# Kernel tuning notes

Hardware: AMD Instinct MI355X
Metric: run time of the kernel (lower is better)

The kernel has to match this reference:

```python
import jax, jax.numpy as jnp
import numpy as np

LN_EPS = 1e-5


def setup_inputs() -> dict:
    key = jax.random.key(0)
    k1, k2 = jax.random.split(key)
    n, c, t, v = 64, 256, 128, 25
    inner2 = 512  # 2 * hidden_dim * n_heads
    return {
        "x": jax.random.normal(k1, (n, c, t, v), dtype=jnp.float32),
        "ln_gamma": jnp.ones((c,), dtype=jnp.float32),
        "ln_beta": jnp.zeros((c,), dtype=jnp.float32),
        "W": jax.random.normal(k2, (inner2, c), dtype=jnp.float32),
        "b": jnp.zeros((inner2,), dtype=jnp.float32),
        "n_heads": 8,
    }


def reference(x, ln_gamma, ln_beta, W, b, n_heads):
    n, c, t, v = x.shape
    inner2 = W.shape[0]
    d = inner2 // 2 // n_heads  # per-head dim
    scale = d ** (-0.5)

    # n c t v -> n t v c
    y = jnp.transpose(x, (0, 2, 3, 1))
    # LayerNorm over channel dim
    mu = jnp.mean(y, axis=-1, keepdims=True)
    var = jnp.mean(jnp.square(y - mu), axis=-1, keepdims=True)
    y = (y - mu) * jax.lax.rsqrt(var + LN_EPS) * ln_gamma + ln_beta
    # QK projection: (n, t, v, 2*h*d)
    y = jnp.einsum('ntvc,ec->ntve', y, W) + b
    q, k = jnp.split(y, 2, axis=-1)

    def heads(z):
        # (n, t, v, h*d) -> (n*t, h, v, d)
        z = z.reshape(n * t, v, n_heads, d)
        return jnp.transpose(z, (0, 2, 1, 3))

    q, k = heads(q), heads(k)
    dots = jnp.einsum('bhid,bhjd->bhij', q, k) * scale
    attn = jax.nn.softmax(dots, axis=-1).astype(jnp.float32)
    return attn
```

## Files before the change

### kernel.cpp

```cpp
#include <hip/hip_runtime.h>
#include <math.h>
#include <stdint.h>

typedef _Float16 f16x8 __attribute__((ext_vector_type(8)));
typedef float    f32x4 __attribute__((ext_vector_type(4)));

#define NB    8192
#define V_    25
#define KS_   0.25505003938643f

__global__ __launch_bounds__(256)
void prep_w(const float* __restrict__ W, _Float16* __restrict__ ws) {
    int tid  = blockIdx.x * 256 + threadIdx.x;
    int lane = tid & 63;
    int idx  = tid >> 6;
    int C    = idx >> 4;
    int T2   = idx & 15;
    int half = C >> 3, ch = C & 7;
    int l15  = lane & 15, q4 = lane >> 4;
    const float* src = W + (size_t)(half*256 + T2*16 + l15) * 256 + ch*32 + q4*8;
    f16x8 hi, lo;
    #pragma unroll
    for (int j = 0; j < 8; ++j) {
        float w = src[j];
        _Float16 hh = (_Float16)w;
        hi[j] = hh;
        lo[j] = (_Float16)(w - (float)hh);
    }
    char* base = (char*)ws + (size_t)idx * 2048 + lane * 16;
    *(f16x8*)base          = hi;
    *(f16x8*)(base + 1024) = lo;
}

struct __align__(16) SMem {
    union {
        float xbuf[256][36];
        struct {
            _Float16 ysh[32][264];
            _Float16 ysl[32][264];
        } g;
        _Float16 qk[4][2][32][72];
    } u;
    float s_mu[32];
    float s_rs[32];
};

__global__ __launch_bounds__(256, 3)
void fused_ln_qk_attn(const float* __restrict__ x,
                      const float* __restrict__ gamma,
                      const float* __restrict__ beta,
                      const _Float16* __restrict__ wsp,
                      const float* __restrict__ bias,
                      float* __restrict__ out)
{
    __shared__ SMem sm;

    const int tid  = threadIdx.x;
    const int lane = tid & 63;
    const int wv   = tid >> 6;
    const int l15  = lane & 15;
    const int q4   = lane >> 4;
    const int nt   = blockIdx.x;
    const int n    = nt >> 7;
    const int t    = nt & 127;
    const int base = n * 819200 + t * 25;

    float xv[32];
    {
        const float* xr = x + base + tid * 3200;
        #pragma unroll
        for (int v = 0; v < V_; ++v) xv[v] = xr[v];
        #pragma unroll
        for (int v = V_; v < 32; ++v) xv[v] = 0.0f;
        #pragma unroll
        for (int i = 0; i < 8; ++i) {
            float4 f;
            f.x = xv[i*4+0]; f.y = xv[i*4+1]; f.z = xv[i*4+2]; f.w = xv[i*4+3];
            *(float4*)&sm.u.xbuf[tid][i*4] = f;
        }
    }
    __syncthreads();

    {
        const int v = tid >> 3;
        const int j = tid & 7;
        float s1 = 0.0f, s2 = 0.0f;
        #pragma unroll 4
        for (int m = 0; m < 32; ++m) {
            float val = sm.u.xbuf[j + 8*m][v];
            s1 += val; s2 += val * val;
        }
        s1 += __shfl_xor(s1, 1); s2 += __shfl_xor(s2, 1);
        s1 += __shfl_xor(s1, 2); s2 += __shfl_xor(s2, 2);
        s1 += __shfl_xor(s1, 4); s2 += __shfl_xor(s2, 4);
        if (j == 0) {
            if (v < V_) {
                float mu  = s1 * (1.0f/256.0f);
                float var = s2 * (1.0f/256.0f) - mu * mu;
                sm.s_mu[v] = mu;
                sm.s_rs[v] = rsqrtf(var + 1e-5f);
            } else { sm.s_mu[v] = 0.0f; sm.s_rs[v] = 0.0f; }
        }
    }
    __syncthreads();

    {
        const float g  = gamma[tid];
        const float be = beta[tid];
        #pragma unroll
        for (int v = 0; v < V_; ++v) {
            float val = (xv[v] - sm.s_mu[v]) * sm.s_rs[v] * g + be;
            _Float16 h = (_Float16)val;
            sm.u.g.ysh[v][tid] = h;
            sm.u.g.ysl[v][tid] = (_Float16)(val - (float)h);
        }
    }
    __syncthreads();

    float bv[2][4];
    #pragma unroll
    for (int h = 0; h < 2; ++h)
        #pragma unroll
        for (int j = 0; j < 4; ++j)
            bv[h][j] = bias[h*256 + (wv*4 + j)*16 + l15];

    f32x4 acc[2][2][4];
    #pragma unroll
    for (int h = 0; h < 2; ++h)
        #pragma unroll
        for (int m = 0; m < 2; ++m)
            #pragma unroll
            for (int j = 0; j < 4; ++j)
                acc[h][m][j] = (f32x4){0.f, 0.f, 0.f, 0.f};

    const char* bbase = (const char*)wsp + (size_t)lane * 16 + (size_t)(wv*4) * 2048;

    for (int ch = 0; ch < 8; ++ch) {
        const int kb = ch*32 + q4*8;
        f16x8 Ah0 = *(const f16x8*)&sm.u.g.ysh[l15][kb];
        f16x8 Ah1 = *(const f16x8*)&sm.u.g.ysh[16 + l15][kb];
        f16x8 Al0 = *(const f16x8*)&sm.u.g.ysl[l15][kb];
        f16x8 Al1 = *(const f16x8*)&sm.u.g.ysl[16 + l15][kb];
        #pragma unroll
        for (int half = 0; half < 2; ++half) {
            const char* cb = bbase + (size_t)(half*8 + ch) * 16 * 2048;
            #pragma unroll
            for (int j = 0; j < 4; ++j) {
                const char* pj = cb + (size_t)j * 2048;
                f16x8 Bh = *(const f16x8*)pj;
                f16x8 Bl = *(const f16x8*)(pj + 1024);
                acc[half][0][j] = __builtin_amdgcn_mfma_f32_16x16x32_f16(Ah0, Bh, acc[half][0][j], 0, 0, 0);
                acc[half][0][j] = __builtin_amdgcn_mfma_f32_16x16x32_f16(Al0, Bh, acc[half][0][j], 0, 0, 0);
                acc[half][0][j] = __builtin_amdgcn_mfma_f32_16x16x32_f16(Ah0, Bl, acc[half][0][j], 0, 0, 0);
                acc[half][1][j] = __builtin_amdgcn_mfma_f32_16x16x32_f16(Ah1, Bh, acc[half][1][j], 0, 0, 0);
                acc[half][1][j] = __builtin_amdgcn_mfma_f32_16x16x32_f16(Al1, Bh, acc[half][1][j], 0, 0, 0);
                acc[half][1][j] = __builtin_amdgcn_mfma_f32_16x16x32_f16(Ah1, Bl, acc[half][1][j], 0, 0, 0);
            }
        }
    }
    __syncthreads();

    #pragma unroll
    for (int hh = 0; hh < 2; ++hh) {
        _Float16 (*qh)[72] = sm.u.qk[wv][0];
        _Float16 (*ql)[72] = sm.u.qk[wv][1];

        #pragma unroll
        for (int half = 0; half < 2; ++half)
            #pragma unroll
            for (int jj = 0; jj < 2; ++jj) {
                const int  j   = 2*hh + jj;
                const float bb = bv[half][j];
                const int  col = half*32 + jj*16 + l15;
                #pragma unroll
                for (int mt = 0; mt < 2; ++mt)
                    #pragma unroll
                    for (int r = 0; r < 4; ++r) {
                        const int row = mt*16 + q4*4 + r;
                        float val  = acc[half][mt][j][r] + bb;
                        _Float16 h = (_Float16)val;
                        qh[row][col] = h;
                        ql[row][col] = (_Float16)(val - (float)h);
                    }
            }

        f16x8 Kh[2], Kl[2], Qh[2], Ql[2];
        #pragma unroll
        for (int tt = 0; tt < 2; ++tt) {
            const int rr = tt*16 + l15;
            Kh[tt] = *(const f16x8*)&qh[rr][32 + q4*8];
            Kl[tt] = *(const f16x8*)&ql[rr][32 + q4*8];
            Qh[tt] = *(const f16x8*)&qh[rr][q4*8];
            Ql[tt] = *(const f16x8*)&ql[rr][q4*8];
        }

        f32x4 D[2][2];
        #pragma unroll
        for (int jt = 0; jt < 2; ++jt)
            #pragma unroll
            for (int it = 0; it < 2; ++it) {
                f32x4 d = (f32x4){0.f, 0.f, 0.f, 0.f};
                d = __builtin_amdgcn_mfma_f32_16x16x32_f16(Kh[jt], Qh[it], d, 0, 0, 0);
                d = __builtin_amdgcn_mfma_f32_16x16x32_f16(Kl[jt], Qh[it], d, 0, 0, 0);
                d = __builtin_amdgcn_mfma_f32_16x16x32_f16(Kh[jt], Ql[it], d, 0, 0, 0);
                D[jt][it] = d;
            }

        float* op = out + (size_t)nt * 5000 + (wv*2 + hh) * 625;
        #pragma unroll
        for (int it = 0; it < 2; ++it) {
            const int i = it*16 + l15;
            float pv[2][4];
            float mx = -3.0e38f;
            #pragma unroll
            for (int jt = 0; jt < 2; ++jt)
                #pragma unroll
                for (int r = 0; r < 4; ++r) {
                    const int j = jt*16 + q4*4 + r;
                    float v = (j < V_) ? D[jt][it][r] : -3.0e38f;
                    pv[jt][r] = v;
                    mx = fmaxf(mx, v);
                }
            mx = fmaxf(mx, __shfl_xor(mx, 16));
            mx = fmaxf(mx, __shfl_xor(mx, 32));
            float sum = 0.0f;
            #pragma unroll
            for (int jt = 0; jt < 2; ++jt)
                #pragma unroll
                for (int r = 0; r < 4; ++r) {
                    float e = exp2f((pv[jt][r] - mx) * KS_);
                    pv[jt][r] = e;
                    sum += e;
                }
            sum += __shfl_xor(sum, 16);
            sum += __shfl_xor(sum, 32);
            const float rcp = 1.0f / sum;
            if (i < V_) {
                #pragma unroll
                for (int jt = 0; jt < 2; ++jt)
                    #pragma unroll
                    for (int r = 0; r < 4; ++r) {
                        const int j = jt*16 + q4*4 + r;
                        if (j < V_) op[i*25 + j] = pv[jt][r] * rcp;
                    }
            }
        }
    }
}

extern "C" void kernel_launch(void* const* d_in, const int* in_sizes, int n_in,
                              void* d_out, int out_size, void* d_ws, size_t ws_size,
                              hipStream_t stream) {
    const float* x     = (const float*)d_in[0];
    const float* gamma = (const float*)d_in[1];
    const float* beta  = (const float*)d_in[2];
    const float* W     = (const float*)d_in[3];
    const float* b     = (const float*)d_in[4];
    _Float16* wsp = (_Float16*)d_ws;
    float* out = (float*)d_out;

    prep_w<<<dim3(64), dim3(256), 0, stream>>>(W, wsp);
    fused_ln_qk_attn<<<dim3(NB), dim3(256), 0, stream>>>(x, gamma, beta, wsp, b, out);
}
```

Measured before the change: 593.0 us.

## Shrink shared memory by staging x as split fp16 and swizzling QK tile

The float32 x staging buffer is dropped. Each input value is now written as an fp16 hi/lo pair straight into the ysh/ysl tiles, and the LayerNorm statistics are computed from vectorised reads of those tiles. The per-wave QK scratch loses its padding and uses an XOR swizzle to avoid bank conflicts, and launch bounds are raised to four blocks per SM. The aim is a smaller LDS footprint for higher occupancy, at the cost of extra conversions, possible register pressure, and statistics computed from split-fp16 values.

```diff
diff --git a/kernel.cpp b/kernel.cpp
--- a/kernel.cpp
+++ b/kernel.cpp
@@ -34,18 +34,17 @@
 
 struct __align__(16) SMem {
     union {
-        float xbuf[256][36];
         struct {
             _Float16 ysh[32][264];
             _Float16 ysl[32][264];
         } g;
-        _Float16 qk[4][2][32][72];
+        _Float16 qk[4][2][32][64];
     } u;
     float s_mu[32];
     float s_rs[32];
 };
 
-__global__ __launch_bounds__(256, 3)
+__global__ __launch_bounds__(256, 4)
 void fused_ln_qk_attn(const float* __restrict__ x,
                       const float* __restrict__ gamma,
                       const float* __restrict__ beta,
@@ -65,18 +64,16 @@
     const int t    = nt & 127;
     const int base = n * 819200 + t * 25;
 
-    float xv[32];
+    float xv[V_];
     {
         const float* xr = x + base + tid * 3200;
         #pragma unroll
         for (int v = 0; v < V_; ++v) xv[v] = xr[v];
         #pragma unroll
-        for (int v = V_; v < 32; ++v) xv[v] = 0.0f;
-        #pragma unroll
-        for (int i = 0; i < 8; ++i) {
-            float4 f;
-            f.x = xv[i*4+0]; f.y = xv[i*4+1]; f.z = xv[i*4+2]; f.w = xv[i*4+3];
-            *(float4*)&sm.u.xbuf[tid][i*4] = f;
+        for (int v = 0; v < V_; ++v) {
+            _Float16 h = (_Float16)xv[v];
+            sm.u.g.ysh[v][tid] = h;
+            sm.u.g.ysl[v][tid] = (_Float16)(xv[v] - (float)h);
         }
     }
     __syncthreads();
@@ -85,10 +82,15 @@
         const int v = tid >> 3;
         const int j = tid & 7;
         float s1 = 0.0f, s2 = 0.0f;
-        #pragma unroll 4
-        for (int m = 0; m < 32; ++m) {
-            float val = sm.u.xbuf[j + 8*m][v];
-            s1 += val; s2 += val * val;
+        #pragma unroll
+        for (int m2 = 0; m2 < 4; ++m2) {
+            f16x8 hv = *(const f16x8*)&sm.u.g.ysh[v][j*32 + m2*8];
+            f16x8 lv = *(const f16x8*)&sm.u.g.ysl[v][j*32 + m2*8];
+            #pragma unroll
+            for (int e = 0; e < 8; ++e) {
+                float val = (float)hv[e] + (float)lv[e];
+                s1 += val; s2 += val * val;
+            }
         }
         s1 += __shfl_xor(s1, 1); s2 += __shfl_xor(s2, 1);
         s1 += __shfl_xor(s1, 2); s2 += __shfl_xor(s2, 2);
@@ -160,11 +162,11 @@
     }
     __syncthreads();
 
+    char* qh = (char*)&sm.u.qk[wv][0][0][0];
+    char* ql = (char*)&sm.u.qk[wv][1][0][0];
+
     #pragma unroll
     for (int hh = 0; hh < 2; ++hh) {
-        _Float16 (*qh)[72] = sm.u.qk[wv][0];
-        _Float16 (*ql)[72] = sm.u.qk[wv][1];
-
         #pragma unroll
         for (int half = 0; half < 2; ++half)
             #pragma unroll
@@ -177,21 +179,25 @@
                     #pragma unroll
                     for (int r = 0; r < 4; ++r) {
                         const int row = mt*16 + q4*4 + r;
+                        const int off = (row*128 + col*2) ^ ((row & 7) << 4);
                         float val  = acc[half][mt][j][r] + bb;
                         _Float16 h = (_Float16)val;
-                        qh[row][col] = h;
-                        ql[row][col] = (_Float16)(val - (float)h);
+                        *(_Float16*)(qh + off) = h;
+                        *(_Float16*)(ql + off) = (_Float16)(val - (float)h);
                     }
             }
 
         f16x8 Kh[2], Kl[2], Qh[2], Ql[2];
         #pragma unroll
         for (int tt = 0; tt < 2; ++tt) {
-            const int rr = tt*16 + l15;
-            Kh[tt] = *(const f16x8*)&qh[rr][32 + q4*8];
-            Kl[tt] = *(const f16x8*)&ql[rr][32 + q4*8];
-            Qh[tt] = *(const f16x8*)&qh[rr][q4*8];
-            Ql[tt] = *(const f16x8*)&ql[rr][q4*8];
+            const int rr  = tt*16 + l15;
+            const int swz = (rr & 7) << 4;
+            const int oK  = (rr*128 + 64 + q4*16) ^ swz;
+            const int oQ  = (rr*128 +      q4*16) ^ swz;
+            Kh[tt] = *(const f16x8*)(qh + oK);
+            Kl[tt] = *(const f16x8*)(ql + oK);
+            Qh[tt] = *(const f16x8*)(qh + oQ);
+            Ql[tt] = *(const f16x8*)(ql + oQ);
         }
 
         f32x4 D[2][2];
```

Result: faster. 542.1 us (-8.6%).
